# Kernel optimization log

Measured on AMD Instinct MI355X. Metric: run time of the kernel, lower is better.

Reference implementation:

```python
import jax, jax.numpy as jnp
import numpy as np

DELTA = 0.04
LOG_CLAMP = -100.0  # torch BCELoss clamps log terms at -100


def setup_inputs() -> dict:
    key = jax.random.key(0)
    k1, k2, k3, k4 = jax.random.split(key, 4)
    B, N = 8192, 2048
    return {
        "anchors": jax.random.normal(k1, (B, N, 2), dtype=jnp.float32),
        "offsets": jax.random.normal(k2, (B, N, 2), dtype=jnp.float32),
        "confidences": jax.random.normal(k3, (B, N), dtype=jnp.float32),
        "ground_truth": jax.random.normal(k4, (B, 2), dtype=jnp.float32),
    }


def _huber_sum(x, delta):
    ax = jnp.abs(x)
    quad = 0.5 * x * x
    lin = delta * (ax - 0.5 * delta)
    return jnp.sum(jnp.where(ax <= delta, quad, lin))


def reference(anchors, offsets, confidences, ground_truth):
    # distances: [B, N] euclidean distance from each anchor to ground truth
    diff = anchors - ground_truth[:, None, :]  # [B, N, 2]
    distances = jnp.sqrt(diff[..., 0] ** 2 + diff[..., 1] ** 2)
    closest_idx = jnp.argmin(distances, axis=-1)  # [B]
    onehot = jax.nn.one_hot(closest_idx, distances.shape[1], dtype=jnp.float32)
    p = jax.nn.softmax(confidences, axis=-1)
    log_p = jnp.maximum(jnp.log(p), LOG_CLAMP)
    log_1mp = jnp.maximum(jnp.log1p(-p), LOG_CLAMP)
    ce_loss = -jnp.sum(onehot * log_p + (1.0 - onehot) * log_1mp)
    # gather closest anchor / offset per batch element
    idx = closest_idx[:, None, None]  # [B,1,1]
    closest_anchors = jnp.take_along_axis(anchors, idx, axis=1)[:, 0, :]  # [B,2]
    closest_offsets = jnp.take_along_axis(offsets, idx, axis=1)[:, 0, :]  # [B,2]
    gt_offset = ground_truth - closest_anchors
    huber_loss = _huber_sum(closest_offsets - gt_offset, DELTA)
    total_loss = ce_loss + huber_loss
    return (total_loss, ce_loss, huber_loss)
```

## Files before the change

### kernel.cpp

```cpp
#include <hip/hip_runtime.h>
#include <math.h>

#define DELTA      0.04f
#define LOG_CLAMP  -100.0f
#define N          2048
#define NPAIR      (N / 2)
#define BLOCK      256
#define KITER      (NPAIR / BLOCK)
#define NWAVES     (BLOCK / 64)

__global__ __launch_bounds__(BLOCK) void row_kernel(
    const float* __restrict__ anchors,
    const float* __restrict__ offsets,
    const float* __restrict__ conf,
    const float* __restrict__ gt,
    float* __restrict__ ce_part,
    float* __restrict__ hu_part)
{
    const int b = blockIdx.x;
    const int t = threadIdx.x;
    const int wid  = t >> 6;
    const int lane = t & 63;

    const float4* __restrict__ arow4 = (const float4*)(anchors + (size_t)b * N * 2);
    const float2* __restrict__ crow2 = (const float2*)(conf + (size_t)b * N);
    const float2 g = ((const float2*)gt)[b];

    __shared__ __attribute__((aligned(16))) float s_exp[N];
    __shared__ float s_f[NWAVES];
    __shared__ float s_s[NWAVES];
    __shared__ int   s_i[NWAVES];
    __shared__ int   s_ci;
    __shared__ float s_inv;

    float dmin = INFINITY;
    int   imin = 0;
    float sume = 0.0f;
    #pragma unroll
    for (int k = 0; k < KITER; ++k) {
        const int q = t + k * BLOCK;
        const float4 a = arow4[q];
        const float2 c = crow2[q];
        const float dx0 = a.x - g.x, dy0 = a.y - g.y;
        const float dx1 = a.z - g.x, dy1 = a.w - g.y;
        const float d0 = dx0 * dx0 + dy0 * dy0;
        const float d1 = dx1 * dx1 + dy1 * dy1;
        if (d0 < dmin) { dmin = d0; imin = 2 * q; }
        if (d1 < dmin) { dmin = d1; imin = 2 * q + 1; }
        const float e0 = __expf(c.x);
        const float e1 = __expf(c.y);
        ((float2*)s_exp)[q] = make_float2(e0, e1);
        sume += e0 + e1;
    }
    #pragma unroll
    for (int off = 32; off > 0; off >>= 1) {
        const float d2 = __shfl_down(dmin, off, 64);
        const int   i2 = __shfl_down(imin, off, 64);
        if (d2 < dmin || (d2 == dmin && i2 < imin)) { dmin = d2; imin = i2; }
        sume += __shfl_down(sume, off, 64);
    }
    if (lane == 0) { s_f[wid] = dmin; s_i[wid] = imin; s_s[wid] = sume; }
    __syncthreads();
    if (t == 0) {
        float bd = s_f[0]; int bi = s_i[0]; float ss = s_s[0];
        #pragma unroll
        for (int w = 1; w < NWAVES; ++w) {
            const float d2 = s_f[w]; const int i2 = s_i[w];
            if (d2 < bd || (d2 == bd && i2 < bi)) { bd = d2; bi = i2; }
            ss += s_s[w];
        }
        s_ci  = bi;
        s_inv = 1.0f / ss;
    }
    __syncthreads();
    const float inv = s_inv;

    float prod = 1.0f;
    #pragma unroll
    for (int k = 0; k < KITER; ++k) {
        const int q = t + k * BLOCK;
        const float2 e = ((const float2*)s_exp)[q];
        prod *= (1.0f - e.x * inv) * (1.0f - e.y * inv);
    }
    float slog = __logf(fmaxf(prod, 1e-37f));
    #pragma unroll
    for (int off = 32; off > 0; off >>= 1)
        slog += __shfl_down(slog, off, 64);
    if (lane == 0) s_s[wid] = slog;
    __syncthreads();

    if (t == 0) {
        float sum_l1mp = 0.0f;
        #pragma unroll
        for (int w = 0; w < NWAVES; ++w) sum_l1mp += s_s[w];

        const int ci = s_ci;
        const float p_ci = s_exp[ci] * inv;
        const float logp_ci = fmaxf(__logf(p_ci),        LOG_CLAMP);
        const float l1mp_ci = fmaxf(__logf(1.0f - p_ci), LOG_CLAMP);
        const float ce = -(logp_ci + (sum_l1mp - l1mp_ci));

        const float2* __restrict__ arow2 = (const float2*)(anchors + (size_t)b * N * 2);
        const float2* __restrict__ orow2 = (const float2*)(offsets + (size_t)b * N * 2);
        const float2 ca = arow2[ci];
        const float2 co = orow2[ci];
        const float x0 = co.x - (g.x - ca.x);
        const float x1 = co.y - (g.y - ca.y);
        const float a0 = fabsf(x0);
        const float a1 = fabsf(x1);
        const float h0 = (a0 <= DELTA) ? 0.5f * x0 * x0 : DELTA * (a0 - 0.5f * DELTA);
        const float h1 = (a1 <= DELTA) ? 0.5f * x1 * x1 : DELTA * (a1 - 0.5f * DELTA);

        ce_part[b] = ce;
        hu_part[b] = h0 + h1;
    }
}

__global__ __launch_bounds__(1024) void reduce_kernel(
    const float* __restrict__ ce_part,
    const float* __restrict__ hu_part,
    float* __restrict__ out, int nrows)
{
    double ce = 0.0, hu = 0.0;
    for (int i = threadIdx.x; i < nrows; i += 1024) {
        ce += (double)ce_part[i];
        hu += (double)hu_part[i];
    }
    #pragma unroll
    for (int off = 32; off > 0; off >>= 1) {
        ce += __shfl_down(ce, off, 64);
        hu += __shfl_down(hu, off, 64);
    }
    __shared__ double sc[16], sh[16];
    const int wid = threadIdx.x >> 6, lane = threadIdx.x & 63;
    if (lane == 0) { sc[wid] = ce; sh[wid] = hu; }
    __syncthreads();
    if (threadIdx.x == 0) {
        double tce = 0.0, thu = 0.0;
        #pragma unroll
        for (int w = 0; w < 16; ++w) { tce += sc[w]; thu += sh[w]; }
        out[0] = (float)(tce + thu);
        out[1] = (float)tce;
        out[2] = (float)thu;
    }
}

extern "C" void kernel_launch(void* const* d_in, const int* in_sizes, int n_in,
                              void* d_out, int out_size, void* d_ws, size_t ws_size,
                              hipStream_t stream) {
    const float* anchors = (const float*)d_in[0];
    const float* offsets = (const float*)d_in[1];
    const float* conf    = (const float*)d_in[2];
    const float* gt      = (const float*)d_in[3];
    float* out = (float*)d_out;

    const int B = in_sizes[3] / 2;

    float* ce_part = (float*)d_ws;
    float* hu_part = ce_part + B;

    row_kernel<<<B, BLOCK, 0, stream>>>(anchors, offsets, conf, gt, ce_part, hu_part);
    reduce_kernel<<<1, 1024, 0, stream>>>(ce_part, hu_part, out, B);
}
```

Baseline: 285.7 us.

## Process one row per wavefront with register-held exponentials instead of shared memory

```diff
diff --git a/kernel.cpp b/kernel.cpp
--- a/kernel.cpp
+++ b/kernel.cpp
@@ -4,10 +4,8 @@
 #define DELTA      0.04f
 #define LOG_CLAMP  -100.0f
 #define N          2048
-#define NPAIR      (N / 2)
 #define BLOCK      256
-#define KITER      (NPAIR / BLOCK)
-#define NWAVES     (BLOCK / 64)
+#define RPB        4
 
 __global__ __launch_bounds__(BLOCK) void row_kernel(
     const float* __restrict__ anchors,
@@ -15,95 +13,77 @@
     const float* __restrict__ conf,
     const float* __restrict__ gt,
     float* __restrict__ ce_part,
-    float* __restrict__ hu_part)
+    float* __restrict__ hu_part,
+    int B)
 {
-    const int b = blockIdx.x;
-    const int t = threadIdx.x;
-    const int wid  = t >> 6;
-    const int lane = t & 63;
+    const int wid  = threadIdx.x >> 6;
+    const int lane = threadIdx.x & 63;
+    const int b = blockIdx.x * RPB + wid;
+    if (b >= B) return;
 
     const float4* __restrict__ arow4 = (const float4*)(anchors + (size_t)b * N * 2);
-    const float2* __restrict__ crow2 = (const float2*)(conf + (size_t)b * N);
+    const float4* __restrict__ crow4 = (const float4*)(conf    + (size_t)b * N);
     const float2 g = ((const float2*)gt)[b];
 
-    __shared__ __attribute__((aligned(16))) float s_exp[N];
-    __shared__ float s_f[NWAVES];
-    __shared__ float s_s[NWAVES];
-    __shared__ int   s_i[NWAVES];
-    __shared__ int   s_ci;
-    __shared__ float s_inv;
+    float e[32];
+    float sume = 0.0f;
+    #pragma unroll
+    for (int k = 0; k < 8; ++k) {
+        const float4 c = crow4[lane + (k << 6)];
+        const float e0 = __expf(c.x), e1 = __expf(c.y);
+        const float e2 = __expf(c.z), e3 = __expf(c.w);
+        e[4*k+0] = e0; e[4*k+1] = e1; e[4*k+2] = e2; e[4*k+3] = e3;
+        sume += (e0 + e1) + (e2 + e3);
+    }
 
     float dmin = INFINITY;
     int   imin = 0;
-    float sume = 0.0f;
     #pragma unroll
-    for (int k = 0; k < KITER; ++k) {
-        const int q = t + k * BLOCK;
+    for (int k = 0; k < 16; ++k) {
+        const int q = lane + (k << 6);
         const float4 a = arow4[q];
-        const float2 c = crow2[q];
         const float dx0 = a.x - g.x, dy0 = a.y - g.y;
         const float dx1 = a.z - g.x, dy1 = a.w - g.y;
         const float d0 = dx0 * dx0 + dy0 * dy0;
         const float d1 = dx1 * dx1 + dy1 * dy1;
-        if (d0 < dmin) { dmin = d0; imin = 2 * q; }
-        if (d1 < dmin) { dmin = d1; imin = 2 * q + 1; }
-        const float e0 = __expf(c.x);
-        const float e1 = __expf(c.y);
-        ((float2*)s_exp)[q] = make_float2(e0, e1);
-        sume += e0 + e1;
+        const int i0 = 2 * q, i1 = 2 * q + 1;
+        if (d0 < dmin || (d0 == dmin && i0 < imin)) { dmin = d0; imin = i0; }
+        if (d1 < dmin || (d1 == dmin && i1 < imin)) { dmin = d1; imin = i1; }
     }
+
     #pragma unroll
     for (int off = 32; off > 0; off >>= 1) {
-        const float d2 = __shfl_down(dmin, off, 64);
-        const int   i2 = __shfl_down(imin, off, 64);
+        const float d2 = __shfl_xor(dmin, off, 64);
+        const int   i2 = __shfl_xor(imin, off, 64);
         if (d2 < dmin || (d2 == dmin && i2 < imin)) { dmin = d2; imin = i2; }
-        sume += __shfl_down(sume, off, 64);
+        sume += __shfl_xor(sume, off, 64);
     }
-    if (lane == 0) { s_f[wid] = dmin; s_i[wid] = imin; s_s[wid] = sume; }
-    __syncthreads();
-    if (t == 0) {
-        float bd = s_f[0]; int bi = s_i[0]; float ss = s_s[0];
-        #pragma unroll
-        for (int w = 1; w < NWAVES; ++w) {
-            const float d2 = s_f[w]; const int i2 = s_i[w];
-            if (d2 < bd || (d2 == bd && i2 < bi)) { bd = d2; bi = i2; }
-            ss += s_s[w];
-        }
-        s_ci  = bi;
-        s_inv = 1.0f / ss;
+    const float inv = 1.0f / sume;
+
+    float p0 = 1.0f, p1 = 1.0f, p2 = 1.0f, p3 = 1.0f;
+    #pragma unroll
+    for (int i = 0; i < 8; ++i) {
+        p0 *= (1.0f - e[4*i+0] * inv);
+        p1 *= (1.0f - e[4*i+1] * inv);
+        p2 *= (1.0f - e[4*i+2] * inv);
+        p3 *= (1.0f - e[4*i+3] * inv);
     }
-    __syncthreads();
-    const float inv = s_inv;
-
-    float prod = 1.0f;
-    #pragma unroll
-    for (int k = 0; k < KITER; ++k) {
-        const int q = t + k * BLOCK;
-        const float2 e = ((const float2*)s_exp)[q];
-        prod *= (1.0f - e.x * inv) * (1.0f - e.y * inv);
-    }
+    const float prod = (p0 * p1) * (p2 * p3);
     float slog = __logf(fmaxf(prod, 1e-37f));
     #pragma unroll
     for (int off = 32; off > 0; off >>= 1)
-        slog += __shfl_down(slog, off, 64);
-    if (lane == 0) s_s[wid] = slog;
-    __syncthreads();
+        slog += __shfl_xor(slog, off, 64);
 
-    if (t == 0) {
-        float sum_l1mp = 0.0f;
-        #pragma unroll
-        for (int w = 0; w < NWAVES; ++w) sum_l1mp += s_s[w];
-
-        const int ci = s_ci;
-        const float p_ci = s_exp[ci] * inv;
+    if (lane == 0) {
+        const int ci = imin;
+        const float e_ci = __expf(conf[(size_t)b * N + ci]);
+        const float p_ci = e_ci * inv;
         const float logp_ci = fmaxf(__logf(p_ci),        LOG_CLAMP);
         const float l1mp_ci = fmaxf(__logf(1.0f - p_ci), LOG_CLAMP);
-        const float ce = -(logp_ci + (sum_l1mp - l1mp_ci));
+        const float ce = -(logp_ci + (slog - l1mp_ci));
 
-        const float2* __restrict__ arow2 = (const float2*)(anchors + (size_t)b * N * 2);
-        const float2* __restrict__ orow2 = (const float2*)(offsets + (size_t)b * N * 2);
-        const float2 ca = arow2[ci];
-        const float2 co = orow2[ci];
+        const float2 ca = ((const float2*)(anchors + (size_t)b * N * 2))[ci];
+        const float2 co = ((const float2*)(offsets + (size_t)b * N * 2))[ci];
         const float x0 = co.x - (g.x - ca.x);
         const float x1 = co.y - (g.y - ca.y);
         const float a0 = fabsf(x0);
@@ -159,6 +139,7 @@
     float* ce_part = (float*)d_ws;
     float* hu_part = ce_part + B;
 
-    row_kernel<<<B, BLOCK, 0, stream>>>(anchors, offsets, conf, gt, ce_part, hu_part);
+    const int grid = (B + RPB - 1) / RPB;
+    row_kernel<<<grid, BLOCK, 0, stream>>>(anchors, offsets, conf, gt, ce_part, hu_part, B);
     reduce_kernel<<<1, 1024, 0, stream>>>(ce_part, hu_part, out, B);
 }
```

Result: slower. 292.9 us (+2.5%).
